# Optimization experiments

Measured on AMD Instinct MI355X. Metric: run time of the kernel, lower is better.

## Reference

```python
import jax, jax.numpy as jnp
import numpy as np

B, T, H = 32, 1000, 512


def setup_inputs() -> dict:
    key = jax.random.key(0)
    k1, k2, k3, k4, k5 = jax.random.split(key, 5)
    return {
        "wx": jax.random.normal(k1, (B, T, 4 * H), dtype=jnp.float32),
        "u": jax.random.normal(k2, (4 * H, H), dtype=jnp.float32) * (1.0 / np.sqrt(H)),
        "u_bias": jax.random.normal(k3, (4 * H,), dtype=jnp.float32) * 0.1,
        "ht": jax.random.normal(k4, (B, H), dtype=jnp.float32),
        "ct": jax.random.normal(k5, (B, H), dtype=jnp.float32),
    }


def reference(wx, u, u_bias, ht, ct):
    # wx: [B, T, 4H]; scan over time with sequential (ht, ct) state.
    def step(carry, wx_t):
        h, c = carry
        gates = wx_t + h @ u.T + u_bias          # [B, 4H]
        it, ft, gt, ot = jnp.split(gates, 4, axis=1)
        it = jax.nn.sigmoid(it)
        ft = jax.nn.sigmoid(ft)
        gt = jnp.tanh(gt)
        ot = jax.nn.sigmoid(ot)
        c = ft * c + it * gt
        h = ot * jnp.tanh(c)
        return (h, c), (h, c, it, ft, gt, ot)

    wx_t = jnp.swapaxes(wx, 0, 1)                # [T, B, 4H]
    _, (h, c, it, ft, gt, ot) = jax.lax.scan(step, (ht, ct), wx_t)
    # each is [T, B, H] -> [B, T, H]
    tr = lambda a: jnp.swapaxes(a, 0, 1)
    return tr(h), tr(c), tr(it), tr(ft), tr(gt), tr(ot)
```

## Files before the change

### kernel.cpp

```cpp
#include <hip/hip_runtime.h>

#define BB 32
#define TT 1000
#define HH 512
#define G4 2048
#define BTH ((size_t)BB * TT * HH)

typedef short short8 __attribute__((ext_vector_type(8)));
typedef float f32x4 __attribute__((ext_vector_type(4)));

__device__ __forceinline__ unsigned short f2bf(float f) {
    union { float f; unsigned u; } v; v.f = f;
    unsigned r = v.u + 0x7FFF + ((v.u >> 16) & 1);
    return (unsigned short)(r >> 16);
}

#define RING_WORDS (2 * 8 * 32 * 64)

__global__ void lstm_init_ring(unsigned* ring) {
    int i = blockIdx.x * 256 + threadIdx.x;
    __hip_atomic_store(ring + i, 0xFFFFFFFFu, __ATOMIC_RELAXED,
                       __HIP_MEMORY_SCOPE_AGENT);
}

#define LDS_BAR() do {                                      \
    asm volatile("s_waitcnt lgkmcnt(0)" ::: "memory");      \
    __builtin_amdgcn_s_barrier();                           \
    asm volatile("" ::: "memory");                          \
    __builtin_amdgcn_sched_barrier(0);                      \
} while (0)

__global__ void __launch_bounds__(256, 1)
lstm_main(const float* __restrict__ wx, const float* __restrict__ u,
          const float* __restrict__ ub, const float* __restrict__ ht0,
          const float* __restrict__ ct0, float* __restrict__ out,
          unsigned* __restrict__ ring)
{
    __shared__ __align__(16) unsigned short lds_h[16 * 512];
    __shared__ float lds_gates[4 * 64];

    const int tid  = threadIdx.x;
    const int bid  = blockIdx.x;
    const int cg   = bid & 31;
    const int qb   = bid >> 5;
    const int lane = tid & 63;
    const int wv   = tid >> 6;

    for (int j = 0; j < 3; ++j) {
        int idx8 = tid + j * 256;
        int r = 4 + (idx8 >> 6);
        int k = (idx8 & 63) * 8;
        short8 z = {0, 0, 0, 0, 0, 0, 0, 0};
        *(short8*)&lds_h[(r * 512 + k) ^ ((r & 7) << 3)] = z;
    }
    {
        int r = wv, k = lane * 8;
        const float* src = ht0 + (size_t)(qb * 4 + r) * HH + k;
        float4 v0 = *(const float4*)src;
        float4 v1 = *(const float4*)(src + 4);
        union { short8 v8; unsigned short s[8]; } p;
        p.s[0] = f2bf(v0.x); p.s[1] = f2bf(v0.y); p.s[2] = f2bf(v0.z); p.s[3] = f2bf(v0.w);
        p.s[4] = f2bf(v1.x); p.s[5] = f2bf(v1.y); p.s[6] = f2bf(v1.z); p.s[7] = f2bf(v1.w);
        *(short8*)&lds_h[(r * 512 + k) ^ ((r & 7) << 3)] = p.v8;
    }

    const int arow = lane & 15, ahi = lane >> 4;
    short8 breg[16];
    {
        const float* bp = u + (size_t)(wv * HH + cg * 16 + arow) * HH + ahi * 8;
#pragma unroll
        for (int kk = 0; kk < 16; ++kk) {
            float4 v0 = *(const float4*)(bp + kk * 32);
            float4 v1 = *(const float4*)(bp + kk * 32 + 4);
            union { short8 v8; unsigned short s[8]; } p;
            p.s[0] = f2bf(v0.x); p.s[1] = f2bf(v0.y); p.s[2] = f2bf(v0.z); p.s[3] = f2bf(v0.w);
            p.s[4] = f2bf(v1.x); p.s[5] = f2bf(v1.y); p.s[6] = f2bf(v1.z); p.s[7] = f2bf(v1.w);
            breg[kk] = p.v8;
        }
    }

    const int gate = lane >> 4;
    const int jc   = lane & 15;
    const float bias_r = ub[gate * HH + cg * 16 + jc];

    float c_reg = 0.f;
    if (lane < 16)
        c_reg = ct0[(size_t)(qb * 4 + wv) * HH + cg * 16 + lane];

    const size_t wx0 = (size_t)(qb * 4 + wv) * TT * G4 + gate * HH + cg * 16 + jc;
    float wx_cur = wx[wx0];
    float wx_nxt = wx[wx0 + G4];

    const size_t ob_gate = (size_t)(2 + gate) * BTH +
                           (size_t)(qb * 4 + wv) * TT * HH + cg * 16 + jc;
    const size_t ob_h = (size_t)(qb * 4 + wv) * TT * HH + cg * 16 + lane;

    const int a_off = arow * 512 + ahi * 8;
    const int a_msk = (arow & 7) << 3;

    const int myp = tid >> 3;
    const int mw  = (tid & 7) * 8;
    const int mb  = mw >> 4;
    const int mj  = mw & 15;

    __syncthreads();

    for (int t = 0; t < TT; ++t) {
        if (t > 0 && myp != cg) {
            const unsigned long long* src = (const unsigned long long*)
                (ring + ((size_t)((t - 1) & 1) * 8 + qb) * 2048 + myp * 64 + mw);
            const unsigned tg = (unsigned)(t - 1);
            const unsigned long long want =
                (unsigned long long)tg | ((unsigned long long)tg << 32);
            const unsigned long long msk = 0x0000FFFF0000FFFFull;
            unsigned long long q0, q1, q2, q3;
            for (;;) {
                q0 = __hip_atomic_load(src + 0, __ATOMIC_RELAXED, __HIP_MEMORY_SCOPE_AGENT);
                q1 = __hip_atomic_load(src + 1, __ATOMIC_RELAXED, __HIP_MEMORY_SCOPE_AGENT);
                q2 = __hip_atomic_load(src + 2, __ATOMIC_RELAXED, __HIP_MEMORY_SCOPE_AGENT);
                q3 = __hip_atomic_load(src + 3, __ATOMIC_RELAXED, __HIP_MEMORY_SCOPE_AGENT);
                if (((q0 & msk) == want) & ((q1 & msk) == want) &
                    ((q2 & msk) == want) & ((q3 & msk) == want)) break;
            }
            union { short8 v8; unsigned u[4]; } pv;
            pv.u[0] = ((unsigned)(q0 >> 16) & 0xFFFFu) | ((unsigned)(q0 >> 48) << 16);
            pv.u[1] = ((unsigned)(q1 >> 16) & 0xFFFFu) | ((unsigned)(q1 >> 48) << 16);
            pv.u[2] = ((unsigned)(q2 >> 16) & 0xFFFFu) | ((unsigned)(q2 >> 48) << 16);
            pv.u[3] = ((unsigned)(q3 >> 16) & 0xFFFFu) | ((unsigned)(q3 >> 48) << 16);
            *(short8*)&lds_h[(mb * 512 + myp * 16 + mj) ^ ((mb & 7) << 3)] = pv.v8;
        }
        LDS_BAR();

        const float wx_use = wx_cur;
        wx_cur = wx_nxt;
        if (t + 2 < TT) wx_nxt = wx[wx0 + (size_t)(t + 2) * G4];

        f32x4 acc0 = {0.f, 0.f, 0.f, 0.f}, acc1 = {0.f, 0.f, 0.f, 0.f};
#pragma unroll
        for (int kk = 0; kk < 8; ++kk) {
            short8 va0 = *(const short8*)&lds_h[(a_off + kk * 32) ^ a_msk];
            short8 va1 = *(const short8*)&lds_h[(a_off + (kk + 8) * 32) ^ a_msk];
            acc0 = __builtin_amdgcn_mfma_f32_16x16x32_bf16(va0, breg[kk], acc0, 0, 0, 0);
            acc1 = __builtin_amdgcn_mfma_f32_16x16x32_bf16(va1, breg[kk + 8], acc1, 0, 0, 0);
        }
        f32x4 g = acc0 + acc1;
        if (lane < 16) {
#pragma unroll
            for (int rr = 0; rr < 4; ++rr)
                lds_gates[rr * 64 + wv * 16 + lane] = g[rr];
        }
        LDS_BAR();

        float gv = lds_gates[wv * 64 + lane] + wx_use + bias_r;
        float xs = (gate == 2) ? 2.f * gv : gv;
        float s  = 1.f / (1.f + __expf(-xs));
        float act = (gate == 2) ? 2.f * s - 1.f : s;

        float af = __shfl(act, (lane & 15) + 16, 64);
        float ag = __shfl(act, (lane & 15) + 32, 64);
        float ao = __shfl(act, (lane & 15) + 48, 64);
        if (lane < 16) {
            c_reg = af * c_reg + act * ag;
            float e2 = __expf(-2.f * c_reg);
            float th = 2.f / (1.f + e2) - 1.f;
            float hn = ao * th;
            unsigned short hb = f2bf(hn);
            unsigned pk = ((unsigned)hb << 16) | (unsigned)t;
            __hip_atomic_store(ring + ((size_t)(t & 1) * 8 + qb) * 2048 +
                                   cg * 64 + wv * 16 + lane,
                               pk, __ATOMIC_RELAXED, __HIP_MEMORY_SCOPE_AGENT);
            lds_h[(wv * 512 + cg * 16 + lane) ^ ((wv & 7) << 3)] = hb;
            out[ob_h + (size_t)t * HH] = hn;
            out[BTH + ob_h + (size_t)t * HH] = c_reg;
        }
        out[ob_gate + (size_t)t * HH] = act;
    }
}

extern "C" void kernel_launch(void* const* d_in, const int* in_sizes, int n_in,
                              void* d_out, int out_size, void* d_ws, size_t ws_size,
                              hipStream_t stream) {
    const float* wx = (const float*)d_in[0];
    const float* u  = (const float*)d_in[1];
    const float* ub = (const float*)d_in[2];
    const float* ht = (const float*)d_in[3];
    const float* ct = (const float*)d_in[4];
    float* out = (float*)d_out;
    unsigned* ring = (unsigned*)d_ws;

    lstm_init_ring<<<RING_WORDS / 256, 256, 0, stream>>>(ring);

    void* args[] = {(void*)&wx, (void*)&u, (void*)&ub, (void*)&ht,
                    (void*)&ct, (void*)&out, (void*)&ring};
    hipLaunchCooperativeKernel((void*)lstm_main, dim3(256), dim3(256), args, 0, stream);
}
```

Baseline: 1.697 ms.

## Replace per-step block barrier with per-slice LDS flag counters and staggered K order

Removes the workgroup barrier before the MFMA loop. Each group of eight threads now bumps an LDS counter for its producer slice after writing it, and each wave waits only on the counters for the K-chunks it is about to consume. Waves start at staggered K offsets so they can begin on whichever parts of h have already arrived. The h and gate LDS buffers are double-buffered, and the block's own slice now also goes through the global ring instead of a direct LDS write. In exchange, the block adds LDS spin-polling and an extra ring round trip for its own data.

After: 2.968 ms. 1.75x slower.

```diff
diff --git a/kernel.cpp b/kernel.cpp
--- a/kernel.cpp
+++ b/kernel.cpp
@@ -36,8 +36,9 @@
           const float* __restrict__ ct0, float* __restrict__ out,
           unsigned* __restrict__ ring)
 {
-    __shared__ __align__(16) unsigned short lds_h[16 * 512];
-    __shared__ float lds_gates[4 * 64];
+    __shared__ __align__(16) unsigned short lds_h[2][16 * 512];
+    __shared__ float lds_gates[2][4 * 64];
+    __shared__ int flagsum[32];
 
     const int tid  = threadIdx.x;
     const int bid  = blockIdx.x;
@@ -46,12 +47,14 @@
     const int lane = tid & 63;
     const int wv   = tid >> 6;
 
-    for (int j = 0; j < 3; ++j) {
+    for (int j = 0; j < 6; ++j) {
         int idx8 = tid + j * 256;
-        int r = 4 + (idx8 >> 6);
-        int k = (idx8 & 63) * 8;
+        int buf  = idx8 >= 768;
+        int r8   = idx8 - buf * 768;
+        int r    = 4 + (r8 >> 6);
+        int k    = (r8 & 63) * 8;
         short8 z = {0, 0, 0, 0, 0, 0, 0, 0};
-        *(short8*)&lds_h[(r * 512 + k) ^ ((r & 7) << 3)] = z;
+        *(short8*)&lds_h[buf][(r * 512 + k) ^ ((r & 7) << 3)] = z;
     }
     {
         int r = wv, k = lane * 8;
@@ -61,7 +64,7 @@
         union { short8 v8; unsigned short s[8]; } p;
         p.s[0] = f2bf(v0.x); p.s[1] = f2bf(v0.y); p.s[2] = f2bf(v0.z); p.s[3] = f2bf(v0.w);
         p.s[4] = f2bf(v1.x); p.s[5] = f2bf(v1.y); p.s[6] = f2bf(v1.z); p.s[7] = f2bf(v1.w);
-        *(short8*)&lds_h[(r * 512 + k) ^ ((r & 7) << 3)] = p.v8;
+        *(short8*)&lds_h[0][(r * 512 + k) ^ ((r & 7) << 3)] = p.v8;
     }
 
     const int arow = lane & 15, ahi = lane >> 4;
@@ -69,13 +72,14 @@
     {
         const float* bp = u + (size_t)(wv * HH + cg * 16 + arow) * HH + ahi * 8;
 #pragma unroll
-        for (int kk = 0; kk < 16; ++kk) {
-            float4 v0 = *(const float4*)(bp + kk * 32);
-            float4 v1 = *(const float4*)(bp + kk * 32 + 4);
+        for (int i = 0; i < 16; ++i) {
+            int kkv = (4 * wv + i) & 15;
+            float4 v0 = *(const float4*)(bp + kkv * 32);
+            float4 v1 = *(const float4*)(bp + kkv * 32 + 4);
             union { short8 v8; unsigned short s[8]; } p;
             p.s[0] = f2bf(v0.x); p.s[1] = f2bf(v0.y); p.s[2] = f2bf(v0.z); p.s[3] = f2bf(v0.w);
             p.s[4] = f2bf(v1.x); p.s[5] = f2bf(v1.y); p.s[6] = f2bf(v1.z); p.s[7] = f2bf(v1.w);
-            breg[kk] = p.v8;
+            breg[i] = p.v8;
         }
     }
 
@@ -103,10 +107,15 @@
     const int mb  = mw >> 4;
     const int mj  = mw & 15;
 
+    if (tid < 32) flagsum[tid] = 0;
+    volatile int* vf = flagsum;
+
     __syncthreads();
 
     for (int t = 0; t < TT; ++t) {
-        if (t > 0 && myp != cg) {
+        const int cur = t & 1;
+
+        if (t > 0) {
             const unsigned long long* src = (const unsigned long long*)
                 (ring + ((size_t)((t - 1) & 1) * 8 + qb) * 2048 + myp * 64 + mw);
             const unsigned tg = (unsigned)(t - 1);
@@ -127,31 +136,48 @@
             pv.u[1] = ((unsigned)(q1 >> 16) & 0xFFFFu) | ((unsigned)(q1 >> 48) << 16);
             pv.u[2] = ((unsigned)(q2 >> 16) & 0xFFFFu) | ((unsigned)(q2 >> 48) << 16);
             pv.u[3] = ((unsigned)(q3 >> 16) & 0xFFFFu) | ((unsigned)(q3 >> 48) << 16);
-            *(short8*)&lds_h[(mb * 512 + myp * 16 + mj) ^ ((mb & 7) << 3)] = pv.v8;
-        }
-        LDS_BAR();
+            *(short8*)&lds_h[cur][(mb * 512 + myp * 16 + mj) ^ ((mb & 7) << 3)] = pv.v8;
+            asm volatile("s_waitcnt lgkmcnt(0)" ::: "memory");
+            __hip_atomic_fetch_add(&flagsum[myp], 1, __ATOMIC_RELAXED,
+                                   __HIP_MEMORY_SCOPE_WORKGROUP);
+        }
 
         const float wx_use = wx_cur;
         wx_cur = wx_nxt;
         if (t + 2 < TT) wx_nxt = wx[wx0 + (size_t)(t + 2) * G4];
 
         f32x4 acc0 = {0.f, 0.f, 0.f, 0.f}, acc1 = {0.f, 0.f, 0.f, 0.f};
+        const int tgt = 8 * t;
 #pragma unroll
-        for (int kk = 0; kk < 8; ++kk) {
-            short8 va0 = *(const short8*)&lds_h[(a_off + kk * 32) ^ a_msk];
-            short8 va1 = *(const short8*)&lds_h[(a_off + (kk + 8) * 32) ^ a_msk];
-            acc0 = __builtin_amdgcn_mfma_f32_16x16x32_bf16(va0, breg[kk], acc0, 0, 0, 0);
-            acc1 = __builtin_amdgcn_mfma_f32_16x16x32_bf16(va1, breg[kk + 8], acc1, 0, 0, 0);
+        for (int i = 0; i < 16; ++i) {
+            if (i == 4 || i == 8 || i == 12) {
+                const int pbase = (8 * wv + 2 * i) & 31;
+                for (;;) {
+                    int m0 = vf[pbase + 0], m1 = vf[pbase + 1];
+                    int m2 = vf[pbase + 2], m3 = vf[pbase + 3];
+                    int m4 = vf[pbase + 4], m5 = vf[pbase + 5];
+                    int m6 = vf[pbase + 6], m7 = vf[pbase + 7];
+                    int mn = min(min(min(m0, m1), min(m2, m3)),
+                                 min(min(m4, m5), min(m6, m7)));
+                    if (mn >= tgt) break;
+                }
+            }
+            const int kk = (4 * wv + i) & 15;
+            short8 a = *(const short8*)&lds_h[cur][(a_off + kk * 32) ^ a_msk];
+            if (i & 1)
+                acc1 = __builtin_amdgcn_mfma_f32_16x16x32_bf16(a, breg[i], acc1, 0, 0, 0);
+            else
+                acc0 = __builtin_amdgcn_mfma_f32_16x16x32_bf16(a, breg[i], acc0, 0, 0, 0);
         }
         f32x4 g = acc0 + acc1;
         if (lane < 16) {
 #pragma unroll
             for (int rr = 0; rr < 4; ++rr)
-                lds_gates[rr * 64 + wv * 16 + lane] = g[rr];
+                lds_gates[cur][rr * 64 + wv * 16 + lane] = g[rr];
         }
         LDS_BAR();
 
-        float gv = lds_gates[wv * 64 + lane] + wx_use + bias_r;
+        float gv = lds_gates[cur][wv * 64 + lane] + wx_use + bias_r;
         float xs = (gate == 2) ? 2.f * gv : gv;
         float s  = 1.f / (1.f + __expf(-xs));
         float act = (gate == 2) ? 2.f * s - 1.f : s;
@@ -169,7 +195,6 @@
             __hip_atomic_store(ring + ((size_t)(t & 1) * 8 + qb) * 2048 +
                                    cg * 64 + wv * 16 + lane,
                                pk, __ATOMIC_RELAXED, __HIP_MEMORY_SCOPE_AGENT);
-            lds_h[(wv * 512 + cg * 16 + lane) ^ ((wv & 7) << 3)] = hb;
             out[ob_h + (size_t)t * HH] = hn;
             out[BTH + ob_h + (size_t)t * HH] = c_reg;
         }
```

## Poll ring via async global-to-LDS loads with double-buffered wavefront checks

Applied to the files above, without the earlier changes.

Replaces the per-thread spinning 64-bit atomic loads of the h-exchange ring with asynchronous global_load_lds requests into a double-buffered LDS poll buffer. Each wave checks eight producer slots with a wave-wide vote. It falls back to plain atomic polling after six attempts, with short sleeps between attempts. The aim is lower cross-block synchronization latency and less memory traffic per timestep, at the cost of extra LDS, more complex ordering with the vmcnt waits, and possible stale reads from the cache policy bits.

Result: slower. 3.105 ms (+83.0%).

```diff
diff --git a/kernel.cpp b/kernel.cpp
--- a/kernel.cpp
+++ b/kernel.cpp
@@ -38,6 +38,7 @@
 {
     __shared__ __align__(16) unsigned short lds_h[16 * 512];
     __shared__ float lds_gates[4 * 64];
+    __shared__ __align__(16) unsigned pollbuf[2][4][8][64];
 
     const int tid  = threadIdx.x;
     const int bid  = blockIdx.x;
@@ -98,36 +99,69 @@
     const int a_off = arow * 512 + ahi * 8;
     const int a_msk = (arow & 7) << 3;
 
-    const int myp = tid >> 3;
-    const int mw  = (tid & 7) * 8;
-    const int mb  = mw >> 4;
-    const int mj  = mw & 15;
-
     __syncthreads();
 
+#define ISSUE_SET(ss) do {                                                    \
+    _Pragma("unroll")                                                         \
+    for (int ii = 0; ii < 8; ++ii) {                                          \
+        const unsigned* gp_ = ring + slotbase + (8 * wv + ii) * 64 + lane;    \
+        __builtin_amdgcn_global_load_lds(                                     \
+            (const __attribute__((address_space(1))) unsigned*)gp_,           \
+            (__attribute__((address_space(3))) unsigned*)&pollbuf[ss][wv][ii][0], \
+            4, 0, 17);                                                        \
+    }                                                                         \
+} while (0)
+
     for (int t = 0; t < TT; ++t) {
-        if (t > 0 && myp != cg) {
-            const unsigned long long* src = (const unsigned long long*)
-                (ring + ((size_t)((t - 1) & 1) * 8 + qb) * 2048 + myp * 64 + mw);
+        if (t > 0) {
+            const unsigned slotbase = ((unsigned)((t - 1) & 1) * 8 + (unsigned)qb) * 2048;
             const unsigned tg = (unsigned)(t - 1);
-            const unsigned long long want =
-                (unsigned long long)tg | ((unsigned long long)tg << 32);
-            const unsigned long long msk = 0x0000FFFF0000FFFFull;
-            unsigned long long q0, q1, q2, q3;
-            for (;;) {
-                q0 = __hip_atomic_load(src + 0, __ATOMIC_RELAXED, __HIP_MEMORY_SCOPE_AGENT);
-                q1 = __hip_atomic_load(src + 1, __ATOMIC_RELAXED, __HIP_MEMORY_SCOPE_AGENT);
-                q2 = __hip_atomic_load(src + 2, __ATOMIC_RELAXED, __HIP_MEMORY_SCOPE_AGENT);
-                q3 = __hip_atomic_load(src + 3, __ATOMIC_RELAXED, __HIP_MEMORY_SCOPE_AGENT);
-                if (((q0 & msk) == want) & ((q1 & msk) == want) &
-                    ((q2 & msk) == want) & ((q3 & msk) == want)) break;
+            unsigned x[8];
+            bool fastok = false;
+            asm volatile("s_waitcnt vmcnt(0)" ::: "memory");
+            __builtin_amdgcn_sched_barrier(0);
+            ISSUE_SET(0);
+            ISSUE_SET(1);
+            int s = 0;
+            for (int chk = 0; chk < 6; ++chk) {
+                asm volatile("s_waitcnt vmcnt(8)" ::: "memory");
+                __builtin_amdgcn_sched_barrier(0);
+#pragma unroll
+                for (int i = 0; i < 8; ++i)
+                    x[i] = *(const volatile unsigned*)&pollbuf[s][wv][i][lane];
+                int ok = 1;
+#pragma unroll
+                for (int i = 0; i < 8; ++i)
+                    if (8 * wv + i != cg) ok &= ((x[i] & 0xFFFFu) == tg);
+                if (__all(ok)) { fastok = true; break; }
+                ISSUE_SET(s);
+                s ^= 1;
+                asm volatile("s_sleep 10" :::);
             }
-            union { short8 v8; unsigned u[4]; } pv;
-            pv.u[0] = ((unsigned)(q0 >> 16) & 0xFFFFu) | ((unsigned)(q0 >> 48) << 16);
-            pv.u[1] = ((unsigned)(q1 >> 16) & 0xFFFFu) | ((unsigned)(q1 >> 48) << 16);
-            pv.u[2] = ((unsigned)(q2 >> 16) & 0xFFFFu) | ((unsigned)(q2 >> 48) << 16);
-            pv.u[3] = ((unsigned)(q3 >> 16) & 0xFFFFu) | ((unsigned)(q3 >> 48) << 16);
-            *(short8*)&lds_h[(mb * 512 + myp * 16 + mj) ^ ((mb & 7) << 3)] = pv.v8;
+            if (!fastok) {
+                for (;;) {
+#pragma unroll
+                    for (int i = 0; i < 8; ++i)
+                        x[i] = __hip_atomic_load(
+                            ring + slotbase + (8 * wv + i) * 64 + lane,
+                            __ATOMIC_RELAXED, __HIP_MEMORY_SCOPE_AGENT);
+                    int ok = 1;
+#pragma unroll
+                    for (int i = 0; i < 8; ++i)
+                        if (8 * wv + i != cg) ok &= ((x[i] & 0xFFFFu) == tg);
+                    if (__all(ok)) break;
+                }
+            }
+            {
+                const int rr = lane >> 4, jj = lane & 15;
+#pragma unroll
+                for (int i = 0; i < 8; ++i) {
+                    const int p = 8 * wv + i;
+                    if (p != cg)
+                        lds_h[(rr * 512 + p * 16 + jj) ^ (rr << 3)] =
+                            (unsigned short)(x[i] >> 16);
+                }
+            }
         }
         LDS_BAR();
 
@@ -175,6 +209,7 @@
         }
         out[ob_gate + (size_t)t * HH] = act;
     }
+#undef ISSUE_SET
 }
 
 extern "C" void kernel_launch(void* const* d_in, const int* in_sizes, int n_in,
```

## Split K across waves and poll ring directly into MFMA A-registers

Applied to the files above, without the earlier changes.

Each wave now computes all four gates over a 128-wide K slice instead of one gate over the full K. Only the lanes holding the four real batch rows poll the global ring, and they pack h straight into MFMA A operands. This removes the LDS h buffer and one of the two per-step barriers, replacing them with a double-buffered LDS partial-sum reduction across the four waves. In exchange the block itself now reads its own h slice back from the ring, and each polling lane issues 16 atomic loads per spin.

New measurement: 2.380 ms. +40.3%, slower.

```diff
diff --git a/kernel.cpp b/kernel.cpp
--- a/kernel.cpp
+++ b/kernel.cpp
@@ -8,6 +8,7 @@
 
 typedef short short8 __attribute__((ext_vector_type(8)));
 typedef float f32x4 __attribute__((ext_vector_type(4)));
+typedef unsigned long long ull;
 
 __device__ __forceinline__ unsigned short f2bf(float f) {
     union { float f; unsigned u; } v; v.f = f;
@@ -36,8 +37,7 @@
           const float* __restrict__ ct0, float* __restrict__ out,
           unsigned* __restrict__ ring)
 {
-    __shared__ __align__(16) unsigned short lds_h[16 * 512];
-    __shared__ float lds_gates[4 * 64];
+    __shared__ __align__(16) float part[2][4][4][16][4];
 
     const int tid  = threadIdx.x;
     const int bid  = blockIdx.x;
@@ -45,37 +45,42 @@
     const int qb   = bid >> 5;
     const int lane = tid & 63;
     const int wv   = tid >> 6;
-
-    for (int j = 0; j < 3; ++j) {
-        int idx8 = tid + j * 256;
-        int r = 4 + (idx8 >> 6);
-        int k = (idx8 & 63) * 8;
-        short8 z = {0, 0, 0, 0, 0, 0, 0, 0};
-        *(short8*)&lds_h[(r * 512 + k) ^ ((r & 7) << 3)] = z;
+    const int arow = lane & 15;
+    const int ahi  = lane >> 4;
+
+    const int woff = arow * 16 + (ahi & 1) * 8;
+    const int p0 = 8 * wv + 0 + (ahi >> 1), p1 = 8 * wv + 2 + (ahi >> 1);
+    const int p2 = 8 * wv + 4 + (ahi >> 1), p3 = 8 * wv + 6 + (ahi >> 1);
+
+    short8 a0 = {0,0,0,0,0,0,0,0}, a1 = a0, a2 = a0, a3 = a0;
+    if (arow < 4) {
+        const float* hp = ht0 + (size_t)(qb * 4 + arow) * HH + 128 * wv + 8 * ahi;
+#define INITA(dst, kk) do {                                                   \
+        float4 v0 = *(const float4*)(hp + (kk) * 32);                         \
+        float4 v1 = *(const float4*)(hp + (kk) * 32 + 4);                     \
+        union { short8 v8; unsigned short s[8]; } p;                          \
+        p.s[0]=f2bf(v0.x); p.s[1]=f2bf(v0.y); p.s[2]=f2bf(v0.z); p.s[3]=f2bf(v0.w); \
+        p.s[4]=f2bf(v1.x); p.s[5]=f2bf(v1.y); p.s[6]=f2bf(v1.z); p.s[7]=f2bf(v1.w); \
+        dst = p.v8; } while (0)
+        INITA(a0, 0); INITA(a1, 1); INITA(a2, 2); INITA(a3, 3);
+#undef INITA
     }
-    {
-        int r = wv, k = lane * 8;
-        const float* src = ht0 + (size_t)(qb * 4 + r) * HH + k;
-        float4 v0 = *(const float4*)src;
-        float4 v1 = *(const float4*)(src + 4);
-        union { short8 v8; unsigned short s[8]; } p;
-        p.s[0] = f2bf(v0.x); p.s[1] = f2bf(v0.y); p.s[2] = f2bf(v0.z); p.s[3] = f2bf(v0.w);
-        p.s[4] = f2bf(v1.x); p.s[5] = f2bf(v1.y); p.s[6] = f2bf(v1.z); p.s[7] = f2bf(v1.w);
-        *(short8*)&lds_h[(r * 512 + k) ^ ((r & 7) << 3)] = p.v8;
-    }
-
-    const int arow = lane & 15, ahi = lane >> 4;
+
     short8 breg[16];
     {
-        const float* bp = u + (size_t)(wv * HH + cg * 16 + arow) * HH + ahi * 8;
 #pragma unroll
-        for (int kk = 0; kk < 16; ++kk) {
-            float4 v0 = *(const float4*)(bp + kk * 32);
-            float4 v1 = *(const float4*)(bp + kk * 32 + 4);
-            union { short8 v8; unsigned short s[8]; } p;
-            p.s[0] = f2bf(v0.x); p.s[1] = f2bf(v0.y); p.s[2] = f2bf(v0.z); p.s[3] = f2bf(v0.w);
-            p.s[4] = f2bf(v1.x); p.s[5] = f2bf(v1.y); p.s[6] = f2bf(v1.z); p.s[7] = f2bf(v1.w);
-            breg[kk] = p.v8;
+        for (int g = 0; g < 4; ++g) {
+            const float* bp = u + (size_t)(g * HH + cg * 16 + arow) * HH +
+                              128 * wv + 8 * ahi;
+#pragma unroll
+            for (int kk = 0; kk < 4; ++kk) {
+                float4 v0 = *(const float4*)(bp + kk * 32);
+                float4 v1 = *(const float4*)(bp + kk * 32 + 4);
+                union { short8 v8; unsigned short s[8]; } p;
+                p.s[0]=f2bf(v0.x); p.s[1]=f2bf(v0.y); p.s[2]=f2bf(v0.z); p.s[3]=f2bf(v0.w);
+                p.s[4]=f2bf(v1.x); p.s[5]=f2bf(v1.y); p.s[6]=f2bf(v1.z); p.s[7]=f2bf(v1.w);
+                breg[g * 4 + kk] = p.v8;
+            }
         }
     }
 
@@ -95,63 +100,81 @@
                            (size_t)(qb * 4 + wv) * TT * HH + cg * 16 + jc;
     const size_t ob_h = (size_t)(qb * 4 + wv) * TT * HH + cg * 16 + lane;
 
-    const int a_off = arow * 512 + ahi * 8;
-    const int a_msk = (arow & 7) << 3;
-
-    const int myp = tid >> 3;
-    const int mw  = (tid & 7) * 8;
-    const int mb  = mw >> 4;
-    const int mj  = mw & 15;
-
     __syncthreads();
 
     for (int t = 0; t < TT; ++t) {
-        if (t > 0 && myp != cg) {
-            const unsigned long long* src = (const unsigned long long*)
-                (ring + ((size_t)((t - 1) & 1) * 8 + qb) * 2048 + myp * 64 + mw);
+        const int cur = t & 1;
+
+        if (t > 0 && arow < 4) {
+            const size_t slotbase = ((size_t)((t - 1) & 1) * 8 + qb) * 2048;
+            const ull* s0 = (const ull*)(ring + slotbase + p0 * 64 + woff);
+            const ull* s1 = (const ull*)(ring + slotbase + p1 * 64 + woff);
+            const ull* s2 = (const ull*)(ring + slotbase + p2 * 64 + woff);
+            const ull* s3 = (const ull*)(ring + slotbase + p3 * 64 + woff);
             const unsigned tg = (unsigned)(t - 1);
-            const unsigned long long want =
-                (unsigned long long)tg | ((unsigned long long)tg << 32);
-            const unsigned long long msk = 0x0000FFFF0000FFFFull;
-            unsigned long long q0, q1, q2, q3;
+            const ull want = (ull)tg | ((ull)tg << 32);
+            const ull msk = 0x0000FFFF0000FFFFull;
+            ull q00,q01,q02,q03, q10,q11,q12,q13, q20,q21,q22,q23, q30,q31,q32,q33;
             for (;;) {
-                q0 = __hip_atomic_load(src + 0, __ATOMIC_RELAXED, __HIP_MEMORY_SCOPE_AGENT);
-                q1 = __hip_atomic_load(src + 1, __ATOMIC_RELAXED, __HIP_MEMORY_SCOPE_AGENT);
-                q2 = __hip_atomic_load(src + 2, __ATOMIC_RELAXED, __HIP_MEMORY_SCOPE_AGENT);
-                q3 = __hip_atomic_load(src + 3, __ATOMIC_RELAXED, __HIP_MEMORY_SCOPE_AGENT);
-                if (((q0 & msk) == want) & ((q1 & msk) == want) &
-                    ((q2 & msk) == want) & ((q3 & msk) == want)) break;
+#define LD4(qa,qb_,qc,qd,sp) do { \
+                qa = __hip_atomic_load(sp+0, __ATOMIC_RELAXED, __HIP_MEMORY_SCOPE_AGENT); \
+                qb_= __hip_atomic_load(sp+1, __ATOMIC_RELAXED, __HIP_MEMORY_SCOPE_AGENT); \
+                qc = __hip_atomic_load(sp+2, __ATOMIC_RELAXED, __HIP_MEMORY_SCOPE_AGENT); \
+                qd = __hip_atomic_load(sp+3, __ATOMIC_RELAXED, __HIP_MEMORY_SCOPE_AGENT); } while (0)
+                LD4(q00,q01,q02,q03, s0); LD4(q10,q11,q12,q13, s1);
+                LD4(q20,q21,q22,q23, s2); LD4(q30,q31,q32,q33, s3);
+#undef LD4
+                bool ok = ((q00&msk)==want)&((q01&msk)==want)&((q02&msk)==want)&((q03&msk)==want)
+                        & ((q10&msk)==want)&((q11&msk)==want)&((q12&msk)==want)&((q13&msk)==want)
+                        & ((q20&msk)==want)&((q21&msk)==want)&((q22&msk)==want)&((q23&msk)==want)
+                        & ((q30&msk)==want)&((q31&msk)==want)&((q32&msk)==want)&((q33&msk)==want);
+                if (ok) break;
             }
-            union { short8 v8; unsigned u[4]; } pv;
-            pv.u[0] = ((unsigned)(q0 >> 16) & 0xFFFFu) | ((unsigned)(q0 >> 48) << 16);
-            pv.u[1] = ((unsigned)(q1 >> 16) & 0xFFFFu) | ((unsigned)(q1 >> 48) << 16);
-            pv.u[2] = ((unsigned)(q2 >> 16) & 0xFFFFu) | ((unsigned)(q2 >> 48) << 16);
-            pv.u[3] = ((unsigned)(q3 >> 16) & 0xFFFFu) | ((unsigned)(q3 >> 48) << 16);
-            *(short8*)&lds_h[(mb * 512 + myp * 16 + mj) ^ ((mb & 7) << 3)] = pv.v8;
-        }
-        LDS_BAR();
+#define PACK(dst, qa,qb_,qc,qd) do {                                          \
+            union { short8 v8; unsigned u[4]; } pv;                           \
+            pv.u[0] = ((unsigned)(qa >> 16) & 0xFFFFu) | ((unsigned)(qa >> 48) << 16); \
+            pv.u[1] = ((unsigned)(qb_>> 16) & 0xFFFFu) | ((unsigned)(qb_>> 48) << 16); \
+            pv.u[2] = ((unsigned)(qc >> 16) & 0xFFFFu) | ((unsigned)(qc >> 48) << 16); \
+            pv.u[3] = ((unsigned)(qd >> 16) & 0xFFFFu) | ((unsigned)(qd >> 48) << 16); \
+            dst = pv.v8; } while (0)
+            PACK(a0, q00,q01,q02,q03); PACK(a1, q10,q11,q12,q13);
+            PACK(a2, q20,q21,q22,q23); PACK(a3, q30,q31,q32,q33);
+#undef PACK
+        }
 
         const float wx_use = wx_cur;
         wx_cur = wx_nxt;
         if (t + 2 < TT) wx_nxt = wx[wx0 + (size_t)(t + 2) * G4];
 
-        f32x4 acc0 = {0.f, 0.f, 0.f, 0.f}, acc1 = {0.f, 0.f, 0.f, 0.f};
-#pragma unroll
-        for (int kk = 0; kk < 8; ++kk) {
-            short8 va0 = *(const short8*)&lds_h[(a_off + kk * 32) ^ a_msk];
-            short8 va1 = *(const short8*)&lds_h[(a_off + (kk + 8) * 32) ^ a_msk];
-            acc0 = __builtin_amdgcn_mfma_f32_16x16x32_bf16(va0, breg[kk], acc0, 0, 0, 0);
-            acc1 = __builtin_amdgcn_mfma_f32_16x16x32_bf16(va1, breg[kk + 8], acc1, 0, 0, 0);
-        }
-        f32x4 g = acc0 + acc1;
+        f32x4 g0 = {0.f,0.f,0.f,0.f}, g1 = g0, g2 = g0, g3 = g0;
+        g0 = __builtin_amdgcn_mfma_f32_16x16x32_bf16(a0, breg[0],  g0, 0, 0, 0);
+        g1 = __builtin_amdgcn_mfma_f32_16x16x32_bf16(a0, breg[4],  g1, 0, 0, 0);
+        g2 = __builtin_amdgcn_mfma_f32_16x16x32_bf16(a0, breg[8],  g2, 0, 0, 0);
+        g3 = __builtin_amdgcn_mfma_f32_16x16x32_bf16(a0, breg[12], g3, 0, 0, 0);
+        g0 = __builtin_amdgcn_mfma_f32_16x16x32_bf16(a1, breg[1],  g0, 0, 0, 0);
+        g1 = __builtin_amdgcn_mfma_f32_16x16x32_bf16(a1, breg[5],  g1, 0, 0, 0);
+        g2 = __builtin_amdgcn_mfma_f32_16x16x32_bf16(a1, breg[9],  g2, 0, 0, 0);
+        g3 = __builtin_amdgcn_mfma_f32_16x16x32_bf16(a1, breg[13], g3, 0, 0, 0);
+        g0 = __builtin_amdgcn_mfma_f32_16x16x32_bf16(a2, breg[2],  g0, 0, 0, 0);
+        g1 = __builtin_amdgcn_mfma_f32_16x16x32_bf16(a2, breg[6],  g1, 0, 0, 0);
+        g2 = __builtin_amdgcn_mfma_f32_16x16x32_bf16(a2, breg[10], g2, 0, 0, 0);
+        g3 = __builtin_amdgcn_mfma_f32_16x16x32_bf16(a2, breg[14], g3, 0, 0, 0);
+        g0 = __builtin_amdgcn_mfma_f32_16x16x32_bf16(a3, breg[3],  g0, 0, 0, 0);
+        g1 = __builtin_amdgcn_mfma_f32_16x16x32_bf16(a3, breg[7],  g1, 0, 0, 0);
+        g2 = __builtin_amdgcn_mfma_f32_16x16x32_bf16(a3, breg[11], g2, 0, 0, 0);
+        g3 = __builtin_amdgcn_mfma_f32_16x16x32_bf16(a3, breg[15], g3, 0, 0, 0);
+
         if (lane < 16) {
-#pragma unroll
-            for (int rr = 0; rr < 4; ++rr)
-                lds_gates[rr * 64 + wv * 16 + lane] = g[rr];
+            *(f32x4*)&part[cur][wv][0][lane][0] = g0;
+            *(f32x4*)&part[cur][wv][1][lane][0] = g1;
+            *(f32x4*)&part[cur][wv][2][lane][0] = g2;
+            *(f32x4*)&part[cur][wv][3][lane][0] = g3;
         }
         LDS_BAR();
 
-        float gv = lds_gates[wv * 64 + lane] + wx_use + bias_r;
+        float gv = part[cur][0][gate][jc][wv] + part[cur][1][gate][jc][wv]
+                 + part[cur][2][gate][jc][wv] + part[cur][3][gate][jc][wv]
+                 + wx_use + bias_r;
         float xs = (gate == 2) ? 2.f * gv : gv;
         float s  = 1.f / (1.f + __expf(-xs));
         float act = (gate == 2) ? 2.f * s - 1.f : s;
@@ -169,7 +192,6 @@
             __hip_atomic_store(ring + ((size_t)(t & 1) * 8 + qb) * 2048 +
                                    cg * 64 + wv * 16 + lane,
                                pk, __ATOMIC_RELAXED, __HIP_MEMORY_SCOPE_AGENT);
-            lds_h[(wv * 512 + cg * 16 + lane) ^ ((wv & 7) << 3)] = hb;
             out[ob_h + (size_t)t * HH] = hn;
             out[BTH + ob_h + (size_t)t * HH] = c_reg;
         }
```
